# Performance work log

Hardware: AMD Instinct MI355X
Metric: run time of the kernel (lower is better)

The kernel has to match this reference:

```python
import jax, jax.numpy as jnp
import numpy as np

B, T, C, H = 2, 2048, 1024, 16
HD = C // H  # head dim = 64


def setup_inputs() -> dict:
    key = jax.random.key(0)
    k1, k2, k3 = jax.random.split(key, 3)
    scale_in = 1.0 / np.sqrt(C)
    x = jax.random.normal(k1, (B, T, C), dtype=jnp.float32)
    w_qkv = jax.random.normal(k2, (C, 3 * C), dtype=jnp.float32) * scale_in
    b_qkv = jnp.zeros((3 * C,), dtype=jnp.float32)
    w_out = jax.random.normal(k3, (C, C), dtype=jnp.float32) * scale_in
    b_out = jnp.zeros((C,), dtype=jnp.float32)
    return {"x": x, "w_qkv": w_qkv, "b_qkv": b_qkv, "w_out": w_out, "b_out": b_out}


def reference(x, w_qkv, b_qkv, w_out, b_out):
    Bq, Tq, Cq = x.shape
    qkv = x @ w_qkv + b_qkv                       # [B,T,3C]
    q, k, v = jnp.split(qkv, 3, axis=-1)          # each [B,T,C]
    # [B,T,C] -> [B,H,T,HD]
    q = q.reshape(Bq, Tq, H, HD).transpose(0, 2, 1, 3)
    k = k.reshape(Bq, Tq, H, HD).transpose(0, 2, 1, 3)
    v = v.reshape(Bq, Tq, H, HD).transpose(0, 2, 1, 3)
    scale = 1.0 / np.sqrt(HD)
    scores = jnp.einsum("bhqd,bhkd->bhqk", q, k) * scale  # [B,H,T,T]
    causal = jnp.tril(jnp.ones((Tq, Tq), dtype=bool))
    scores = jnp.where(causal[None, None], scores, jnp.finfo(scores.dtype).min)
    attn = jax.nn.softmax(scores, axis=-1)
    y = jnp.einsum("bhqk,bhkd->bhqd", attn, v)    # [B,H,T,HD]
    y = y.transpose(0, 2, 1, 3).reshape(Bq, Tq, Cq)
    return y @ w_out + b_out
```

## Files before the change

### kernel.cpp

```cpp
#include <hip/hip_runtime.h>
#include <hip/hip_bf16.h>


#define B_ 2
#define T_ 2048
#define C_ 1024
#define H_ 16
#define HD_ 64
#define M_ (B_ * T_)
#define N3_ (3 * C_)
#define QK2_ 2048
#define QSCALE 0.18033688f

typedef __attribute__((ext_vector_type(8))) short short8;
typedef __attribute__((ext_vector_type(4))) short short4v;
typedef __attribute__((ext_vector_type(4))) float floatx4;

__device__ __forceinline__ unsigned short f2b(float f) {
    __hip_bfloat16 h = __float2bfloat16(f);
    return *reinterpret_cast<unsigned short*>(&h);
}

__device__ __forceinline__ float fexp2(float x) {
#if __has_builtin(__builtin_amdgcn_exp2f)
    return __builtin_amdgcn_exp2f(x);
#else
    return exp2f(x);
#endif
}

__device__ __forceinline__ void glds16(const void* g, void* l) {
    __builtin_amdgcn_global_load_lds(
        (const __attribute__((address_space(1))) void*)g,
        (__attribute__((address_space(3))) void*)l, 16, 0, 0);
}

__global__ __launch_bounds__(256) void prep(
    const float* __restrict__ x, const float* __restrict__ w_qkv,
    const float* __restrict__ w_out, unsigned short* __restrict__ xb,
    unsigned short* __restrict__ wt1, unsigned short* __restrict__ wt2) {
    __shared__ float t[64][33];
    const int bi = blockIdx.x;
    const int tid = threadIdx.x;
    if (bi < 4096) {
        int i = (bi * 256 + tid) * 4;
        float4 v = *reinterpret_cast<const float4*>(x + i);
        short4v s;
        s[0] = (short)f2b(v.x); s[1] = (short)f2b(v.y);
        s[2] = (short)f2b(v.z); s[3] = (short)f2b(v.w);
        *reinterpret_cast<short4v*>(xb + i) = s;
        return;
    }
    const float* src; unsigned short* dst; int n0, k0, N;
    if (bi < 4096 + 1536) {
        int u = bi - 4096;
        src = w_qkv; dst = wt1; N = N3_;
        k0 = (u & 15) * 64; n0 = (u >> 4) * 32;
    } else {
        int u = bi - (4096 + 1536);
        src = w_out; dst = wt2; N = C_;
        k0 = (u & 15) * 64; n0 = (u >> 4) * 32;
    }
    const int tx = tid & 31, ty = tid >> 5;
#pragma unroll
    for (int i = 0; i < 8; i++)
        t[ty + i * 8][tx] = src[(size_t)(k0 + ty + i * 8) * N + n0 + tx];
    __syncthreads();
    const int row = tid >> 3;
    const int kp  = (tid & 7) * 8;
    short8 o;
#pragma unroll
    for (int j = 0; j < 8; j++) o[j] = (short)f2b(t[kp + j][row]);
    *reinterpret_cast<short8*>(&dst[(size_t)(n0 + row) * C_ + k0 + kp]) = o;
}

template<int EPI, int BN>
__global__ __launch_bounds__(256) void gemm_glds(
    const unsigned short* __restrict__ A, const unsigned short* __restrict__ Bt,
    const float* __restrict__ bias, void* __restrict__ Cp,
    unsigned short* __restrict__ vtp, int M, int N, int K) {
    constexpr int NI = BN / 32;
    __shared__ __align__(16) unsigned short Al[128 * 64];
    __shared__ __align__(16) unsigned short Bl[BN * 64];

    const int tid  = threadIdx.x;
    const int lane = tid & 63;
    const int w    = tid >> 6;
    const int c16  = lane & 15;
    const int quad = lane >> 4;
    const int NT  = N / BN;
    const int pe  = NT >> 3;
    const int xcd = blockIdx.x & 7;
    const int ii  = blockIdx.x >> 3;
    const int n0  = (xcd * pe + ii % pe) * BN;
    const int m0  = (ii / pe) * 128;
    const int wm = (w >> 1) * 64;
    const int wn = (w & 1) * (BN / 2);

    floatx4 acc[4][NI] = {};

    const int srow = lane >> 3;
    const int sch  = ((lane & 7) ^ srow) * 8;
    const unsigned short* ag = A + (size_t)(m0 + w * 32 + srow) * K + sch;
    const unsigned short* bg = Bt + (size_t)(n0 + w * (BN / 4) + srow) * K + sch;

    const int s7 = c16 & 7;

    for (int k0 = 0; k0 < K; k0 += 64) {
        __syncthreads();
#pragma unroll
        for (int i = 0; i < 4; i++)
            glds16(ag + k0 + (size_t)(i * 8) * K, &Al[(w * 32 + i * 8) * 64]);
#pragma unroll
        for (int i = 0; i < BN / 32; i++)
            glds16(bg + k0 + (size_t)(i * 8) * K,
                   &Bl[(w * (BN / 4) + i * 8) * 64]);
        __syncthreads();

        short8 af[4][2], bf[NI][2];
#pragma unroll
        for (int im = 0; im < 4; im++)
#pragma unroll
            for (int kk = 0; kk < 2; kk++)
                af[im][kk] = *reinterpret_cast<const short8*>(
                    &Al[(wm + im * 16 + c16) * 64 + ((kk * 4 + quad) ^ s7) * 8]);
#pragma unroll
        for (int in = 0; in < NI; in++)
#pragma unroll
            for (int kk = 0; kk < 2; kk++)
                bf[in][kk] = *reinterpret_cast<const short8*>(
                    &Bl[(wn + in * 16 + c16) * 64 + ((kk * 4 + quad) ^ s7) * 8]);
#pragma unroll
        for (int im = 0; im < 4; im++)
#pragma unroll
            for (int in = 0; in < NI; in++)
#pragma unroll
                for (int kk = 0; kk < 2; kk++)
                    acc[im][in] = __builtin_amdgcn_mfma_f32_16x16x32_bf16(
                        af[im][kk], bf[in][kk], acc[im][in], 0, 0, 0);
    }

    const int ncol = n0 + wn;
    float bv[NI];
#pragma unroll
    for (int in = 0; in < NI; in++) bv[in] = bias[ncol + in * 16 + c16];

    if (EPI == 0) {
        float* C = (float*)Cp;
#pragma unroll
        for (int im = 0; im < 4; im++)
#pragma unroll
            for (int r = 0; r < 4; r++) {
                int row = m0 + wm + im * 16 + quad * 4 + r;
#pragma unroll
                for (int in = 0; in < NI; in++)
                    C[(size_t)row * N + ncol + in * 16 + c16] =
                        acc[im][in][r] + bv[in];
            }
    } else {
        if (ncol < 2 * C_) {
            const float fac = (ncol < C_) ? QSCALE : 1.0f;
            unsigned short* qkp = (unsigned short*)Cp;
#pragma unroll
            for (int im = 0; im < 4; im++)
#pragma unroll
                for (int r = 0; r < 4; r++) {
                    int row = m0 + wm + im * 16 + quad * 4 + r;
#pragma unroll
                    for (int in = 0; in < NI; in++)
                        qkp[(size_t)row * QK2_ + ncol + in * 16 + c16] =
                            f2b((acc[im][in][r] + bv[in]) * fac);
                }
        } else {
#pragma unroll
            for (int im = 0; im < 4; im++) {
                int row0 = m0 + wm + im * 16 + quad * 4;
                int b  = row0 >> 11;
                int t0 = row0 & (T_ - 1);
#pragma unroll
                for (int in = 0; in < NI; in++) {
                    int dfull = ncol - 2 * C_ + in * 16 + c16;
                    short4v sv;
#pragma unroll
                    for (int r = 0; r < 4; r++)
                        sv[r] = (short)f2b(acc[im][in][r] + bv[in]);
                    *reinterpret_cast<short4v*>(
                        &vtp[(((size_t)(b << 10) + dfull) << 11) + t0]) = sv;
                }
            }
        }
    }
}

__global__ __launch_bounds__(256) void repack(
    const unsigned short* __restrict__ qk, const unsigned short* __restrict__ vt,
    unsigned short* __restrict__ kfb, unsigned short* __restrict__ vfb) {
    const int bh    = blockIdx.x >> 5;
    const int chunk = blockIdx.x & 31;
    const int b = bh >> 4, h = bh & 15;
    const int tid  = threadIdx.x;
    const int frag = tid >> 5;
    const int ll0  = (tid & 31) * 2;
    const size_t obase = ((size_t)(bh * 32 + chunk)) * 4096 + frag * 512;

    {
        const int ws = frag >> 2, sub = (frag >> 1) & 1, dh = frag & 1;
#pragma unroll
        for (int e = 0; e < 2; e++) {
            const int ll = ll0 + e, quad = ll >> 4, c16 = ll & 15;
            const int key = chunk * 64 + ws * 32 + sub * 16 + c16;
            short8 v = *reinterpret_cast<const short8*>(
                qk + ((size_t)(b * T_ + key)) * QK2_ + C_ + h * HD_ +
                dh * 32 + quad * 8);
            *reinterpret_cast<short8*>(kfb + obase + ll * 8) = v;
        }
    }
    {
        const int ws = frag >> 2, dt = frag & 3;
#pragma unroll
        for (int e = 0; e < 2; e++) {
            const int ll = ll0 + e, quad = ll >> 4, c16 = ll & 15;
            const int d = dt * 16 + c16;
            const unsigned short* src = vt + ((size_t)(bh * 64 + d)) * T_ +
                                        chunk * 64 + ws * 32 + quad * 4;
            short4v v0 = *reinterpret_cast<const short4v*>(src);
            short4v v1 = *reinterpret_cast<const short4v*>(src + 16);
            short8 o;
            o[0] = v0[0]; o[1] = v0[1]; o[2] = v0[2]; o[3] = v0[3];
            o[4] = v1[0]; o[5] = v1[1]; o[6] = v1[2]; o[7] = v1[3];
            *reinterpret_cast<short8*>(vfb + obase + ll * 8) = o;
        }
    }
}

#define ATTN_CHUNK(MASKED, kb, kcp, vcp)                                      \
{                                                                             \
    short8 kf00 = *reinterpret_cast<const short8*>((kcp));                    \
    short8 kf01 = *reinterpret_cast<const short8*>((kcp) + 512);              \
    short8 kf10 = *reinterpret_cast<const short8*>((kcp) + 1024);             \
    short8 kf11 = *reinterpret_cast<const short8*>((kcp) + 1536);             \
    short8 vf[4];                                                             \
    _Pragma("unroll")                                                         \
    for (int dt = 0; dt < 4; dt++)                                            \
        vf[dt] = *reinterpret_cast<const short8*>((vcp) + dt * 512);          \
    short8 pf[2];                                                             \
    _Pragma("unroll")                                                         \
    for (int qt = 0; qt < 2; qt++) {                                          \
        floatx4 s0 = __builtin_amdgcn_mfma_f32_16x16x32_bf16(                 \
            kf00, af[qt][0], z, 0, 0, 0);                                     \
        s0 = __builtin_amdgcn_mfma_f32_16x16x32_bf16(                         \
            kf01, af[qt][1], s0, 0, 0, 0);                                    \
        floatx4 s1 = __builtin_amdgcn_mfma_f32_16x16x32_bf16(                 \
            kf10, af[qt][0], z, 0, 0, 0);                                     \
        s1 = __builtin_amdgcn_mfma_f32_16x16x32_bf16(                         \
            kf11, af[qt][1], s1, 0, 0, 0);                                    \
        short8 p8;                                                            \
        _Pragma("unroll")                                                     \
        for (int r = 0; r < 4; r++) {                                         \
            float p0, p1;                                                     \
            if (MASKED) {                                                     \
                int key0 = (kb) + ws * 32 + quad * 4 + r;                     \
                int qr = q0 + wq * 32 + qt * 16 + c16;                        \
                p0 = (key0 <= qr) ? fexp2(s0[r]) : 0.f;                       \
                p1 = (key0 + 16 <= qr) ? fexp2(s1[r]) : 0.f;                  \
            } else {                                                          \
                p0 = fexp2(s0[r]);                                            \
                p1 = fexp2(s1[r]);                                            \
            }                                                                 \
            p8[r] = (short)f2b(p0);                                           \
            p8[4 + r] = (short)f2b(p1);                                       \
        }                                                                     \
        pf[qt] = p8;                                                          \
    }                                                                         \
    _Pragma("unroll")                                                         \
    for (int qt = 0; qt < 2; qt++)                                            \
        O1[qt] = __builtin_amdgcn_mfma_f32_16x16x32_bf16(                     \
            pf[qt], ones, O1[qt], 0, 0, 0);                                   \
    _Pragma("unroll")                                                         \
    for (int dt = 0; dt < 4; dt++)                                            \
        _Pragma("unroll")                                                     \
        for (int qt = 0; qt < 2; qt++)                                        \
            O[qt][dt] = __builtin_amdgcn_mfma_f32_16x16x32_bf16(              \
                pf[qt], vf[dt], O[qt][dt], 0, 0, 0);                          \
}

__global__ __launch_bounds__(256, 3) void attn_mfma(
    const unsigned short* __restrict__ qk,
    const unsigned short* __restrict__ kfb,
    const unsigned short* __restrict__ vfb,
    unsigned short* __restrict__ y) {
    __shared__ __align__(16) float Of[4096];
    __shared__ __align__(16) float Lb[1024];

    const int tid  = threadIdx.x;
    const int lane = tid & 63;
    const int w    = tid >> 6;
    const int wq   = w & 1;
    const int ws   = w >> 1;
    const int c16  = lane & 15;
    const int quad = lane >> 4;
    const int bh = blockIdx.x & 31;
    const int t  = 31 - (blockIdx.x >> 5);
    const int b  = bh >> 4;
    const int h  = bh & 15;
    const int q0 = t * 64;
    const int nch = t + 1;

    const unsigned short* qrow = qk + (size_t)b * T_ * QK2_ + h * HD_;
    const unsigned short* kfp = kfb + ((size_t)bh * 32) * 4096 + ws * 2048 + lane * 8;
    const unsigned short* vfp = vfb + ((size_t)bh * 32) * 4096 + ws * 2048 + lane * 8;

    short8 af[2][2];
#pragma unroll
    for (int qt = 0; qt < 2; qt++)
#pragma unroll
        for (int hh = 0; hh < 2; hh++)
            af[qt][hh] = *reinterpret_cast<const short8*>(
                qrow + (size_t)(q0 + wq * 32 + qt * 16 + c16) * QK2_ +
                hh * 32 + quad * 8);

    floatx4 O[2][4] = {};
    floatx4 O1[2] = {};
    const floatx4 z = {0.f, 0.f, 0.f, 0.f};
    short8 ones;
#pragma unroll
    for (int j = 0; j < 8; j++) ones[j] = (short)0x3F80;

    for (int c = 0; c < nch; c++) {
        const int kb = c * 64;
        const unsigned short* kcp = kfp + (size_t)c * 4096;
        const unsigned short* vcp = vfp + (size_t)c * 4096;
        if (c + 1 < nch) {
            ATTN_CHUNK(0, kb, kcp, vcp)
        } else if (!(wq == 0 && ws == 1)) {
            ATTN_CHUNK(1, kb, kcp, vcp)
        }
    }

    if (ws) {
#pragma unroll
        for (int qt = 0; qt < 2; qt++) {
#pragma unroll
            for (int dt = 0; dt < 4; dt++)
                *reinterpret_cast<floatx4*>(
                    &Of[wq * 2048 + qt * 1024 + dt * 256 + lane * 4]) = O[qt][dt];
            *reinterpret_cast<floatx4*>(
                &Lb[wq * 512 + qt * 256 + lane * 4]) = O1[qt];
        }
    }
    __syncthreads();
    if (ws == 0) {
#pragma unroll
        for (int qt = 0; qt < 2; qt++) {
#pragma unroll
            for (int dt = 0; dt < 4; dt++)
                O[qt][dt] += *reinterpret_cast<const floatx4*>(
                    &Of[wq * 2048 + qt * 1024 + dt * 256 + lane * 4]);
            floatx4 lr = O1[qt] + *reinterpret_cast<const floatx4*>(
                    &Lb[wq * 512 + qt * 256 + lane * 4]);

#pragma unroll
            for (int dt = 0; dt < 4; dt++)
#pragma unroll
                for (int r = 0; r < 4; r++) {
                    float val = O[qt][dt][r] / fmaxf(lr[r], 1e-30f);
                    y[((size_t)b * T_ + q0 + wq * 32 + qt * 16 + quad * 4 + r)
                          * C_ + h * HD_ + dt * 16 + c16] = f2b(val);
                }
        }
    }
}

extern "C" void kernel_launch(void* const* d_in, const int* in_sizes, int n_in,
                              void* d_out, int out_size, void* d_ws, size_t ws_size,
                              hipStream_t stream) {
    const float* x     = (const float*)d_in[0];
    const float* w_qkv = (const float*)d_in[1];
    const float* b_qkv = (const float*)d_in[2];
    const float* w_out = (const float*)d_in[3];
    const float* b_out = (const float*)d_in[4];
    float* out = (float*)d_out;

    unsigned short* qkb = (unsigned short*)d_ws;
    unsigned short* vtb = qkb + (size_t)M_ * QK2_;
    unsigned short* yb  = vtb + (size_t)B_ * H_ * HD_ * T_;
    unsigned short* wt1 = yb + (size_t)M_ * C_;
    unsigned short* wt2 = wt1 + (size_t)N3_ * C_;
    unsigned short* xb  = wt2 + (size_t)C_ * C_;
    unsigned short* kfb = xb + (size_t)M_ * C_;
    unsigned short* vfb = kfb + (size_t)32 * 32 * 4096;

    prep<<<4096 + 1536 + 512, 256, 0, stream>>>(x, w_qkv, w_out, xb, wt1, wt2);

    gemm_glds<1, 128><<<(N3_ / 128) * (M_ / 128), 256, 0, stream>>>(
        xb, wt1, b_qkv, qkb, vtb, M_, N3_, C_);

    repack<<<32 * 32, 256, 0, stream>>>(qkb, vtb, kfb, vfb);

    attn_mfma<<<B_ * H_ * 32, 256, 0, stream>>>(qkb, kfb, vfb, yb);

    gemm_glds<0, 64><<<(C_ / 64) * (M_ / 128), 256, 0, stream>>>(
        yb, wt2, b_out, out, nullptr, M_, C_, C_);
}
```

Baseline: 179.9 us.

## Fuse K/V fragment repacking into QKV GEMM epilogue, drop repack kernel

Result: faster. 172.2 us (-4.3%).

```diff
diff --git a/kernel.cpp b/kernel.cpp
--- a/kernel.cpp
+++ b/kernel.cpp
@@ -9,7 +9,6 @@
 #define HD_ 64
 #define M_ (B_ * T_)
 #define N3_ (3 * C_)
-#define QK2_ 2048
 #define QSCALE 0.18033688f
 
 typedef __attribute__((ext_vector_type(8))) short short8;
@@ -78,7 +77,8 @@
 __global__ __launch_bounds__(256) void gemm_glds(
     const unsigned short* __restrict__ A, const unsigned short* __restrict__ Bt,
     const float* __restrict__ bias, void* __restrict__ Cp,
-    unsigned short* __restrict__ vtp, int M, int N, int K) {
+    unsigned short* __restrict__ kfbp, unsigned short* __restrict__ vfbp,
+    int M, int N, int K) {
     constexpr int NI = BN / 32;
     __shared__ __align__(16) unsigned short Al[128 * 64];
     __shared__ __align__(16) unsigned short Bl[BN * 64];
@@ -158,9 +158,8 @@
                         acc[im][in][r] + bv[in];
             }
     } else {
-        if (ncol < 2 * C_) {
-            const float fac = (ncol < C_) ? QSCALE : 1.0f;
-            unsigned short* qkp = (unsigned short*)Cp;
+        if (ncol < C_) {
+            unsigned short* qb = (unsigned short*)Cp;
 #pragma unroll
             for (int im = 0; im < 4; im++)
 #pragma unroll
@@ -168,67 +167,61 @@
                     int row = m0 + wm + im * 16 + quad * 4 + r;
 #pragma unroll
                     for (int in = 0; in < NI; in++)
-                        qkp[(size_t)row * QK2_ + ncol + in * 16 + c16] =
-                            f2b((acc[im][in][r] + bv[in]) * fac);
+                        qb[(size_t)row * C_ + ncol + in * 16 + c16] =
+                            f2b((acc[im][in][r] + bv[in]) * QSCALE);
                 }
-        } else {
+        } else if (ncol < 2 * C_) {
 #pragma unroll
             for (int im = 0; im < 4; im++) {
                 int row0 = m0 + wm + im * 16 + quad * 4;
-                int b  = row0 >> 11;
-                int t0 = row0 & (T_ - 1);
+                int b    = row0 >> 11;
+                int key  = row0 & (T_ - 1);
+                int chunk = key >> 6;
+                int kk    = key & 63;
+                int wsd   = kk >> 5;
+                int subd  = (kk >> 4) & 1;
+                int c16d  = kk & 15;
+#pragma unroll
+                for (int in = 0; in < NI; in++) {
+                    int dfull = ncol - C_ + in * 16 + c16;
+                    int hh = dfull >> 6;
+                    int d  = dfull & 63;
+                    size_t base =
+                        ((size_t)((b * 16 + hh) * 32 + chunk)) * 4096 +
+                        (wsd * 4 + subd * 2 + (d >> 5)) * 512 +
+                        (((d >> 3) & 3) * 16 + c16d) * 8 + (d & 7);
+#pragma unroll
+                    for (int r = 0; r < 4; r++)
+                        kfbp[base + (size_t)r * 8] =
+                            f2b(acc[im][in][r] + bv[in]);
+                }
+            }
+        } else {
+#pragma unroll
+            for (int im = 0; im < 4; im++) {
+                int row0 = m0 + wm + im * 16 + quad * 4;
+                int b    = row0 >> 11;
+                int key  = row0 & (T_ - 1);
+                int chunk = key >> 6;
+                int kk    = key & 63;
+                int wsd   = kk >> 5;
+                int qd    = (kk >> 2) & 3;
+                int jb    = (kk & 16) ? 4 : 0;
 #pragma unroll
                 for (int in = 0; in < NI; in++) {
                     int dfull = ncol - 2 * C_ + in * 16 + c16;
+                    int hh = dfull >> 6;
+                    int d  = dfull & 63;
                     short4v sv;
 #pragma unroll
                     for (int r = 0; r < 4; r++)
                         sv[r] = (short)f2b(acc[im][in][r] + bv[in]);
                     *reinterpret_cast<short4v*>(
-                        &vtp[(((size_t)(b << 10) + dfull) << 11) + t0]) = sv;
+                        &vfbp[((size_t)((b * 16 + hh) * 32 + chunk)) * 4096 +
+                              (wsd * 4 + (d >> 4)) * 512 +
+                              (qd * 16 + (d & 15)) * 8 + jb]) = sv;
                 }
             }
-        }
-    }
-}
-
-__global__ __launch_bounds__(256) void repack(
-    const unsigned short* __restrict__ qk, const unsigned short* __restrict__ vt,
-    unsigned short* __restrict__ kfb, unsigned short* __restrict__ vfb) {
-    const int bh    = blockIdx.x >> 5;
-    const int chunk = blockIdx.x & 31;
-    const int b = bh >> 4, h = bh & 15;
-    const int tid  = threadIdx.x;
-    const int frag = tid >> 5;
-    const int ll0  = (tid & 31) * 2;
-    const size_t obase = ((size_t)(bh * 32 + chunk)) * 4096 + frag * 512;
-
-    {
-        const int ws = frag >> 2, sub = (frag >> 1) & 1, dh = frag & 1;
-#pragma unroll
-        for (int e = 0; e < 2; e++) {
-            const int ll = ll0 + e, quad = ll >> 4, c16 = ll & 15;
-            const int key = chunk * 64 + ws * 32 + sub * 16 + c16;
-            short8 v = *reinterpret_cast<const short8*>(
-                qk + ((size_t)(b * T_ + key)) * QK2_ + C_ + h * HD_ +
-                dh * 32 + quad * 8);
-            *reinterpret_cast<short8*>(kfb + obase + ll * 8) = v;
-        }
-    }
-    {
-        const int ws = frag >> 2, dt = frag & 3;
-#pragma unroll
-        for (int e = 0; e < 2; e++) {
-            const int ll = ll0 + e, quad = ll >> 4, c16 = ll & 15;
-            const int d = dt * 16 + c16;
-            const unsigned short* src = vt + ((size_t)(bh * 64 + d)) * T_ +
-                                        chunk * 64 + ws * 32 + quad * 4;
-            short4v v0 = *reinterpret_cast<const short4v*>(src);
-            short4v v1 = *reinterpret_cast<const short4v*>(src + 16);
-            short8 o;
-            o[0] = v0[0]; o[1] = v0[1]; o[2] = v0[2]; o[3] = v0[3];
-            o[4] = v1[0]; o[5] = v1[1]; o[6] = v1[2]; o[7] = v1[3];
-            *reinterpret_cast<short8*>(vfb + obase + ll * 8) = o;
         }
     }
 }
@@ -306,7 +299,7 @@
     const int q0 = t * 64;
     const int nch = t + 1;
 
-    const unsigned short* qrow = qk + (size_t)b * T_ * QK2_ + h * HD_;
+    const unsigned short* qrow = qk + (size_t)b * T_ * C_ + h * HD_;
     const unsigned short* kfp = kfb + ((size_t)bh * 32) * 4096 + ws * 2048 + lane * 8;
     const unsigned short* vfp = vfb + ((size_t)bh * 32) * 4096 + ws * 2048 + lane * 8;
 
@@ -316,7 +309,7 @@
 #pragma unroll
         for (int hh = 0; hh < 2; hh++)
             af[qt][hh] = *reinterpret_cast<const short8*>(
-                qrow + (size_t)(q0 + wq * 32 + qt * 16 + c16) * QK2_ +
+                qrow + (size_t)(q0 + wq * 32 + qt * 16 + c16) * C_ +
                 hh * 32 + quad * 8);
 
     floatx4 O[2][4] = {};
@@ -381,24 +374,21 @@
     const float* b_out = (const float*)d_in[4];
     float* out = (float*)d_out;
 
-    unsigned short* qkb = (unsigned short*)d_ws;
-    unsigned short* vtb = qkb + (size_t)M_ * QK2_;
-    unsigned short* yb  = vtb + (size_t)B_ * H_ * HD_ * T_;
+    unsigned short* qb  = (unsigned short*)d_ws;
+    unsigned short* kfb = qb + (size_t)M_ * C_;
+    unsigned short* vfb = kfb + (size_t)32 * 32 * 4096;
+    unsigned short* yb  = vfb + (size_t)32 * 32 * 4096;
     unsigned short* wt1 = yb + (size_t)M_ * C_;
     unsigned short* wt2 = wt1 + (size_t)N3_ * C_;
     unsigned short* xb  = wt2 + (size_t)C_ * C_;
-    unsigned short* kfb = xb + (size_t)M_ * C_;
-    unsigned short* vfb = kfb + (size_t)32 * 32 * 4096;
 
     prep<<<4096 + 1536 + 512, 256, 0, stream>>>(x, w_qkv, w_out, xb, wt1, wt2);
 
     gemm_glds<1, 128><<<(N3_ / 128) * (M_ / 128), 256, 0, stream>>>(
-        xb, wt1, b_qkv, qkb, vtb, M_, N3_, C_);
-
-    repack<<<32 * 32, 256, 0, stream>>>(qkb, vtb, kfb, vfb);
-
-    attn_mfma<<<B_ * H_ * 32, 256, 0, stream>>>(qkb, kfb, vfb, yb);
+        xb, wt1, b_qkv, qb, kfb, vfb, M_, N3_, C_);
+
+    attn_mfma<<<B_ * H_ * 32, 256, 0, stream>>>(qb, kfb, vfb, yb);
 
     gemm_glds<0, 64><<<(C_ / 64) * (M_ / 128), 256, 0, stream>>>(
-        yb, wt2, b_out, out, nullptr, M_, C_, C_);
-}
+        yb, wt2, b_out, out, nullptr, nullptr, M_, C_, C_);
+}
```
